# Kernel optimization log

Measured on AMD Instinct MI355X. Metric: run time of the kernel, lower is better.

Reference implementation:

```python
import jax, jax.numpy as jnp
import numpy as np

B, L, D, C, N, K = 4096, 4096, 1024, 64, 8192, 5
TEMP = 0.1
ALPHA = 2.0
EPS = 1e-12


def setup_inputs() -> dict:
    key = jax.random.key(0)
    ks = jax.random.split(key, 8)
    x = jax.random.normal(ks[0], (B, 1, L), jnp.float32)
    y = jax.random.randint(ks[1], (B,), 0, C)
    Wf = jax.random.normal(ks[2], (L, D), jnp.float32) * 0.02
    Wc = jax.random.normal(ks[3], (C, D), jnp.float32) * 0.02
    bc = jnp.zeros((C,), jnp.float32)
    supports_old = jax.random.normal(ks[4], (N, D), jnp.float32)
    scores_old = jax.nn.softmax(jax.random.normal(ks[5], (N, C), jnp.float32), axis=-1)
    labels_old = jax.nn.one_hot(jax.random.randint(ks[6], (N,), 0, C), C, dtype=jnp.float32)
    return dict(x=x, y=y, Wf=Wf, Wc=Wc, bc=bc, supports_old=supports_old,
                labels_old=labels_old, scores_old=scores_old)


def _l2n(v, axis):
    return v / jnp.maximum(jnp.linalg.norm(v, axis=axis, keepdims=True), EPS)


def _masked_mean(v, w):
    return jnp.sum(v * w) / jnp.maximum(jnp.sum(w), 1.0)


def _tta_loss(x, Wf, Wc, bc, supports_old, labels_old, scores_old):
    feats = x.reshape(B, L) @ Wf                      # [B, D] featurizer
    logits = feats @ Wc.T + bc                        # [B, C]
    probs = jax.nn.softmax(logits, -1)
    logp = jax.nn.log_softmax(logits, -1)
    prob = probs.max(-1)
    pred = jnp.argmax(logits, -1)
    # prediction-confidence filter
    y_certain = prob >= prob.mean()
    # input-energy entropy filter (scipy.stats.entropy over axis=2)
    px = x * x
    px = px / jnp.maximum(px.sum(2, keepdims=True), EPS)
    e = -(px * jnp.log(px + 1e-30)).sum(2).reshape(B)
    e_certain = e < e.mean()
    w_c = (e_certain & y_certain).astype(jnp.float32)  # certain mask as weights
    w_u = 1.0 - w_c
    yhat = jax.nn.one_hot(pred, C, dtype=jnp.float32)
    # --- memory bank concat + prototype build (no_grad in torch) ---
    sup_all = jnp.concatenate([supports_old, feats], 0)        # [N+B, D]
    lab_all = jnp.concatenate([labels_old, yhat], 0)           # [N+B, C]
    w_all = jnp.concatenate([jnp.ones((N,), jnp.float32), w_c], 0)
    lw = lab_all * w_all[:, None]
    protos = _l2n(sup_all, 1).T @ lw / jnp.maximum(lw.sum(0, keepdims=True), EPS)
    protos = jax.lax.stop_gradient(_l2n(protos, 0))            # [D, C]
    # --- loss1: Tsallis entropy - diversity on balanced probs ---
    m = jnp.sum(probs * w_c[:, None], 0) / jnp.maximum(w_c.sum(), 1.0)
    pb = probs / jnp.maximum(m, EPS)
    pb = pb / pb.sum(1, keepdims=True)
    tsallis = jnp.mean((1.0 - jnp.sum(pb ** ALPHA, 1)) / (ALPHA - 1.0))
    pm = pb.mean(0)
    div = -jnp.sum(pm * jnp.log(pm + EPS))
    loss1 = tsallis - div
    # --- loss2: PCL, prototype CE on certain samples (temp=1) ---
    lp = jax.nn.log_softmax(_l2n(feats, 1) @ protos, -1)       # [B, C]
    ce = -jnp.take_along_axis(lp, pred[:, None], 1)[:, 0]
    loss2 = _masked_mean(ce, w_c)
    # --- loss3: NCL, kNN soft targets from memory bank, uncertain rows ---
    scores_all = jax.lax.stop_gradient(jnp.concatenate([scores_old, probs], 0))
    sup_det = jax.lax.stop_gradient(sup_all)
    sim = _l2n(feats, 1) @ _l2n(sup_det, 1).T / TEMP           # [B, N+B]
    sim = jnp.where(w_all[None, :] > 0, sim, -jnp.inf)
    _, idx = jax.lax.top_k(sim, K)                             # [B, K]
    tgt = scores_all[idx].mean(1)                              # [B, C]
    ncl = -(tgt * logp).sum(1)
    loss3 = _masked_mean(ncl, w_u)
    return loss1 + loss2 + loss3


def reference(x, y, Wf, Wc, bc, supports_old, labels_old, scores_old):
    return _tta_loss(x, Wf, Wc, bc, supports_old, labels_old, scores_old)
```

## Files before the change

### kernel.cpp

```cpp
#include <hip/hip_runtime.h>
#include <math.h>

#define BBATCH 4096
#define LLEN   4096
#define DDIM   1024
#define CCLS   64
#define NSUP   8192
#define NTOT   12288
#define FEPS   1e-12f
#define KCHUNK 96
#define KCAND  (KCHUNK*5)

#define SC_SUMP  0
#define SC_SUME  1
#define SC_SUMWC 2
#define SC_TSAL  3
#define SC_L2NUM 4
#define SC_L3NUM 5

typedef _Float16 half4_t __attribute__((ext_vector_type(4)));
typedef _Float16 half8_t __attribute__((ext_vector_type(8)));
typedef float    f32x4   __attribute__((ext_vector_type(4)));
typedef float    f32x16  __attribute__((ext_vector_type(16)));

static const size_t OFF_FEATS  = 0;
static const size_t OFF_FEATP1 = OFF_FEATS  + (size_t)BBATCH*DDIM;
static const size_t OFF_WFTH   = OFF_FEATP1 + (size_t)BBATCH*DDIM;
static const size_t OFF_WFTL   = OFF_WFTH   + (size_t)DDIM*LLEN/2;
static const size_t OFF_PROBS  = OFF_WFTL   + (size_t)DDIM*LLEN/2;
static const size_t OFF_LOGP   = OFF_PROBS  + (size_t)BBATCH*CCLS;
static const size_t OFF_FNORM  = OFF_LOGP   + (size_t)BBATCH*CCLS;
static const size_t OFF_SNORM  = OFF_FNORM  + BBATCH;
static const size_t OFF_PMAX   = OFF_SNORM  + NSUP;
static const size_t OFF_EROW   = OFF_PMAX   + BBATCH;
static const size_t OFF_WC     = OFF_EROW   + BBATCH;
static const size_t OFF_PRED   = OFF_WC     + BBATCH;
static const size_t OFF_RB     = OFF_PRED   + BBATCH;
static const size_t OFF_SNM    = OFF_RB     + BBATCH;
static const size_t OFF_PROTOT = OFF_SNM    + NTOT;
static const size_t OFF_CVAL   = OFF_PROTOT + (size_t)CCLS*DDIM;
static const size_t OFF_CIDX   = OFF_CVAL   + (size_t)BBATCH*KCAND;
static const size_t OFF_ZERO   = OFF_CIDX   + (size_t)BBATCH*KCAND;
static const size_t OFF_MACC   = OFF_ZERO;
static const size_t OFF_PMACC  = OFF_MACC   + CCLS;
static const size_t OFF_COLS   = OFF_PMACC  + CCLS;
static const size_t OFF_SCAL   = OFF_COLS   + CCLS;
static const size_t OFF_PROTUN = OFF_SCAL   + 32;
static const size_t OFF_ZEND   = OFF_PROTUN + (size_t)DDIM*CCLS;
static const size_t OFF_SUPH   = OFF_ZEND;
static const size_t OFF_SUPL   = OFF_SUPH   + (size_t)NSUP*DDIM/2;
static const size_t WS_END     = OFF_SUPL   + (size_t)NSUP*DDIM/2;

__device__ __forceinline__ float waveSum(float v){
  #pragma unroll
  for (int o = 32; o > 0; o >>= 1) v += __shfl_xor(v, o);
  return v;
}
__device__ __forceinline__ float waveMax(float v){
  #pragma unroll
  for (int o = 32; o > 0; o >>= 1) v = fmaxf(v, __shfl_xor(v, o));
  return v;
}
__device__ __forceinline__ float blockSum256(float v, float* sh4){
  v = waveSum(v);
  if ((threadIdx.x & 63) == 0) sh4[threadIdx.x >> 6] = v;
  __syncthreads();
  float r = sh4[0] + sh4[1] + sh4[2] + sh4[3];
  __syncthreads();
  return r;
}
__device__ __forceinline__ void top5_insert(float* v, int* ix, float s, int si){
  bool c0 = s > v[0], c1 = s > v[1], c2 = s > v[2], c3 = s > v[3], c4 = s > v[4];
  v[4] = c4 ? (c3 ? v[3] : s) : v[4];  ix[4] = c4 ? (c3 ? ix[3] : si) : ix[4];
  v[3] = c3 ? (c2 ? v[2] : s) : v[3];  ix[3] = c3 ? (c2 ? ix[2] : si) : ix[3];
  v[2] = c2 ? (c1 ? v[1] : s) : v[2];  ix[2] = c2 ? (c1 ? ix[1] : si) : ix[2];
  v[1] = c1 ? (c0 ? v[0] : s) : v[1];  ix[1] = c1 ? (c0 ? ix[0] : si) : ix[1];
  v[0] = c0 ? s : v[0];                ix[0] = c0 ? si : ix[0];
}
__device__ __forceinline__ void split4(const float4 v, half4_t* h, half4_t* l){
  half4_t hh, ll;
  hh[0] = (_Float16)v.x; hh[1] = (_Float16)v.y; hh[2] = (_Float16)v.z; hh[3] = (_Float16)v.w;
  ll[0] = (_Float16)(v.x - (float)hh[0]);
  ll[1] = (_Float16)(v.y - (float)hh[1]);
  ll[2] = (_Float16)(v.z - (float)hh[2]);
  ll[3] = (_Float16)(v.w - (float)hh[3]);
  *h = hh; *l = ll;
}

__global__ __launch_bounds__(256)
void k_entropy(const float* __restrict__ x, float* __restrict__ e_row,
               float* __restrict__ scal){
  __shared__ __align__(16) float lx[LLEN];
  __shared__ float sh4[4];
  int row = blockIdx.x, t = threadIdx.x;
  const float4* xr = (const float4*)(x + (size_t)row * LLEN);
  float s = 0.f;
  #pragma unroll
  for (int i = 0; i < 4; ++i){
    float4 v = xr[t + 256*i];
    ((float4*)lx)[t + 256*i] = v;
    s += v.x*v.x + v.y*v.y + v.z*v.z + v.w*v.w;
  }
  s = blockSum256(s, sh4);
  float inv = 1.0f / fmaxf(s, FEPS);
  float ent = 0.f;
  #pragma unroll
  for (int i = 0; i < 4; ++i){
    float4 v = ((float4*)lx)[t + 256*i];
    float p;
    p = v.x*v.x*inv; ent -= p * logf(p + 1e-30f);
    p = v.y*v.y*inv; ent -= p * logf(p + 1e-30f);
    p = v.z*v.z*inv; ent -= p * logf(p + 1e-30f);
    p = v.w*v.w*inv; ent -= p * logf(p + 1e-30f);
  }
  ent = blockSum256(ent, sh4);
  if (t == 0){ e_row[row] = ent; atomicAdd(&scal[SC_SUME], ent); }
}

__global__ __launch_bounds__(256)
void k_wft(const float* __restrict__ Wf, unsigned short* __restrict__ WftH,
           unsigned short* __restrict__ WftL){
  __shared__ __align__(16) float ld[64*68];
  int t = threadIdx.x;
  int d0 = blockIdx.x * 64;
  int l0 = blockIdx.y * 64;
  #pragma unroll
  for (int i = 0; i < 4; ++i){
    int flat = t + 256*i;
    int l = flat >> 4, d4 = (flat & 15) * 4;
    *(float4*)&ld[l*68 + d4] = *(const float4*)(Wf + (size_t)(l0+l)*DDIM + d0 + d4);
  }
  __syncthreads();
  #pragma unroll
  for (int i = 0; i < 4; ++i){
    int flat = t + 256*i;
    int d = flat >> 4, l4 = (flat & 15) * 4;
    float4 v = make_float4(ld[(l4+0)*68 + d], ld[(l4+1)*68 + d],
                           ld[(l4+2)*68 + d], ld[(l4+3)*68 + d]);
    half4_t h, l;
    split4(v, &h, &l);
    *(half4_t*)(WftH + (size_t)(d0+d)*LLEN + l0 + l4) = h;
    *(half4_t*)(WftL + (size_t)(d0+d)*LLEN + l0 + l4) = l;
  }
}

#define LP 40
__global__ __launch_bounds__(256)
void k_feats_mfma(const float* __restrict__ X, const unsigned short* __restrict__ WftH,
                  const unsigned short* __restrict__ WftL, float* __restrict__ featp){
  __shared__ __align__(16) _Float16 lds[4*128*LP];
  _Float16* Ah = lds;
  _Float16* Al = lds + 128*LP;
  _Float16* Bh = lds + 2*128*LP;
  _Float16* Bl = lds + 3*128*LP;
  int t = threadIdx.x;
  int n0 = blockIdx.x * 128;
  int m0 = blockIdx.y * 128;
  int kz = blockIdx.z;
  int w = t >> 6, lane = t & 63;
  int wr = w >> 1, wc = w & 1;
  int lr = lane & 15, lg = lane >> 4;
  int ar = t >> 3, akq = (t & 7);
  int br = t >> 2, bk8 = (t & 3) * 8;
  f32x4 acc[4][4];
  #pragma unroll
  for (int i=0;i<4;++i){
    #pragma unroll
    for (int j=0;j<4;++j) acc[i][j] = (f32x4)(0.f);
  }
  const int kend = kz*2048 + 2048;
  float4 avs[4]; uint4 bhs[2], bls[2];
  {
    int k0 = kz*2048;
    #pragma unroll
    for (int i=0;i<4;++i)
      avs[i] = *(const float4*)(X + (size_t)(m0 + ar + 32*i)*LLEN + k0 + akq*4);
    #pragma unroll
    for (int i=0;i<2;++i){
      bhs[i] = *(const uint4*)(WftH + (size_t)(n0 + br + 64*i)*LLEN + k0 + bk8);
      bls[i] = *(const uint4*)(WftL + (size_t)(n0 + br + 64*i)*LLEN + k0 + bk8);
    }
  }
  for (int k0 = kz*2048; k0 < kend; k0 += 32){
    __syncthreads();
    #pragma unroll
    for (int i=0;i<4;++i){
      half4_t h, l;
      split4(avs[i], &h, &l);
      *(half4_t*)&Ah[(ar + 32*i)*LP + akq*4] = h;
      *(half4_t*)&Al[(ar + 32*i)*LP + akq*4] = l;
    }
    #pragma unroll
    for (int i=0;i<2;++i){
      *(uint4*)&Bh[(br + 64*i)*LP + bk8] = bhs[i];
      *(uint4*)&Bl[(br + 64*i)*LP + bk8] = bls[i];
    }
    __syncthreads();
    if (k0 + 32 < kend){
      int kn = k0 + 32;
      #pragma unroll
      for (int i=0;i<4;++i)
        avs[i] = *(const float4*)(X + (size_t)(m0 + ar + 32*i)*LLEN + kn + akq*4);
      #pragma unroll
      for (int i=0;i<2;++i){
        bhs[i] = *(const uint4*)(WftH + (size_t)(n0 + br + 64*i)*LLEN + kn + bk8);
        bls[i] = *(const uint4*)(WftL + (size_t)(n0 + br + 64*i)*LLEN + kn + bk8);
      }
    }
    half8_t ah[4], al[4], bh[4], bl[4];
    #pragma unroll
    for (int mi=0;mi<4;++mi){
      const _Float16* p = &Ah[(wr*64 + mi*16 + lr)*LP + lg*8];
      ah[mi] = *(const half8_t*)p;
      al[mi] = *(const half8_t*)(p + 128*LP);
    }
    #pragma unroll
    for (int ni=0;ni<4;++ni){
      const _Float16* p = &Bh[(wc*64 + ni*16 + lr)*LP + lg*8];
      bh[ni] = *(const half8_t*)p;
      bl[ni] = *(const half8_t*)(p + 128*LP);
    }
    #pragma unroll
    for (int mi=0;mi<4;++mi){
      #pragma unroll
      for (int ni=0;ni<4;++ni){
        acc[mi][ni] = __builtin_amdgcn_mfma_f32_16x16x32_f16(ah[mi], bh[ni], acc[mi][ni], 0,0,0);
        acc[mi][ni] = __builtin_amdgcn_mfma_f32_16x16x32_f16(ah[mi], bl[ni], acc[mi][ni], 0,0,0);
        acc[mi][ni] = __builtin_amdgcn_mfma_f32_16x16x32_f16(al[mi], bh[ni], acc[mi][ni], 0,0,0);
      }
    }
  }
  float* outp = featp + (size_t)kz * BBATCH * DDIM;
  #pragma unroll
  for (int mi=0;mi<4;++mi){
    #pragma unroll
    for (int ni=0;ni<4;++ni){
      #pragma unroll
      for (int r=0;r<4;++r){
        int row = m0 + wr*64 + mi*16 + lg*4 + r;
        int col = n0 + wc*64 + ni*16 + lr;
        outp[(size_t)row*DDIM + col] = acc[mi][ni][r];
      }
    }
  }
}

__global__ __launch_bounds__(256)
void k_supnorm(const float* __restrict__ sup, float* __restrict__ snorm,
               _Float16* __restrict__ suph, _Float16* __restrict__ supl){
  int w = threadIdx.x >> 6, lane = threadIdx.x & 63;
  int row = blockIdx.x*4 + w;
  const float4* rp = (const float4*)(sup + (size_t)row * DDIM);
  float s = 0.f;
  #pragma unroll
  for (int j=0;j<4;++j){
    float4 v = rp[lane + 64*j];
    half4_t h, l;
    split4(v, &h, &l);
    *(half4_t*)(suph + (size_t)row*DDIM + (lane + 64*j)*4) = h;
    *(half4_t*)(supl + (size_t)row*DDIM + (lane + 64*j)*4) = l;
    s += v.x*v.x+v.y*v.y+v.z*v.z+v.w*v.w;
  }
  s = waveSum(s);
  if (lane==0) snorm[row] = sqrtf(s);
}

__global__ __launch_bounds__(256)
void k_logits(float* __restrict__ feats, const float* __restrict__ featp1,
              const float* __restrict__ Wc,
              const float* __restrict__ bc, float* __restrict__ probs,
              float* __restrict__ logp, float* __restrict__ pmax,
              int* __restrict__ pred, float* __restrict__ fnorm,
              float* __restrict__ scal,
              _Float16* __restrict__ fh, _Float16* __restrict__ fl){
  __shared__ __align__(16) float f[DDIM];
  __shared__ float z[CCLS];
  __shared__ float sh4[4];
  int row = blockIdx.x, t = threadIdx.x;
  const float4* fr0 = (const float4*)(feats  + (size_t)row * DDIM);
  const float4* fr1 = (const float4*)(featp1 + (size_t)row * DDIM);
  float ss = 0.f;
  { float4 a = fr0[t], b = fr1[t];
    float4 v = make_float4(a.x+b.x, a.y+b.y, a.z+b.z, a.w+b.w);
    ((float4*)f)[t] = v;
    ((float4*)(feats + (size_t)row*DDIM))[t] = v;
    half4_t h, l;
    split4(v, &h, &l);
    *(half4_t*)(fh + (size_t)row*DDIM + t*4) = h;
    *(half4_t*)(fl + (size_t)row*DDIM + t*4) = l;
    ss += v.x*v.x+v.y*v.y+v.z*v.z+v.w*v.w; }
  ss = blockSum256(ss, sh4);
  if (t==0) fnorm[row] = sqrtf(ss);
  int w = t >> 6, lane = t & 63;
  for (int ci = 0; ci < 16; ++ci){
    int c = w*16 + ci;
    const float4* wc = (const float4*)(Wc + (size_t)c * DDIM);
    float d = 0.f;
    #pragma unroll
    for (int j=0;j<4;++j){
      float4 a = wc[lane + 64*j];
      float4 b = ((float4*)f)[lane + 64*j];
      d += a.x*b.x+a.y*b.y+a.z*b.z+a.w*b.w;
    }
    d = waveSum(d);
    if (lane == 0) z[c] = d + bc[c];
  }
  __syncthreads();
  if (w == 0){
    float zz = z[lane];
    float m = waveMax(zz);
    unsigned long long bal = __ballot(zz == m);
    int am = __ffsll(bal) - 1;
    float ex = expf(zz - m);
    float sv = waveSum(ex);
    probs[(size_t)row*CCLS + lane] = ex / sv;
    logp[(size_t)row*CCLS + lane]  = (zz - m) - logf(sv);
    if (lane == 0){
      float pmv = 1.0f / sv;
      pmax[row] = pmv;
      pred[row] = am;
      atomicAdd(&scal[SC_SUMP], pmv);
    }
  }
}

__global__ __launch_bounds__(256)
void k_mask(const float* __restrict__ e_row, const float* __restrict__ pmax,
            const float* __restrict__ fnorm, const float* __restrict__ snorm,
            const int* __restrict__ pred, float* __restrict__ w_c,
            float* __restrict__ rb, float* __restrict__ snm,
            float* __restrict__ colsum, float* __restrict__ scal){
  int i = blockIdx.x * 256 + threadIdx.x;
  if (i < NSUP) snm[i] = 1.0f / fmaxf(snorm[i], FEPS);
  if (i < BBATCH){
    float me = scal[SC_SUME] * (1.0f/BBATCH);
    float mp = scal[SC_SUMP] * (1.0f/BBATCH);
    float wc = ((e_row[i] < me) && (pmax[i] >= mp)) ? 1.0f : 0.0f;
    w_c[i] = wc;
    float fn = fmaxf(fnorm[i], FEPS);
    rb[i] = 10.0f / fn;
    snm[NSUP + i] = (wc > 0.f) ? (1.0f / fn) : -1.0f;
    atomicAdd(&scal[SC_SUMWC], wc);
    atomicAdd(&colsum[pred[i]], wc);
  }
}

__global__ __launch_bounds__(256)
void k_colsum_labels(const float* __restrict__ labels, float* __restrict__ colsum){
  int t = threadIdx.x, c = t & 63, sub = t >> 6;
  int r0 = blockIdx.x * 256;
  float s = 0.f;
  for (int i = 0; i < 64; ++i){
    int r = r0 + sub + 4*i;
    s += labels[(size_t)r*CCLS + c];
  }
  __shared__ float loc[4][64];
  loc[sub][c] = s;
  __syncthreads();
  if (sub == 0) atomicAdd(&colsum[c], loc[0][c]+loc[1][c]+loc[2][c]+loc[3][c]);
}

__global__ __launch_bounds__(256)
void k_m_accum(const float* __restrict__ probs, const float* __restrict__ w_c,
               float* __restrict__ m_acc){
  int t = threadIdx.x, c = t & 63, sub = t >> 6;
  int r0 = blockIdx.x * 64;
  float s = 0.f;
  for (int i = 0; i < 16; ++i){
    int r = r0 + sub + 4*i;
    s += probs[(size_t)r*CCLS + c] * w_c[r];
  }
  __shared__ float loc[4][64];
  loc[sub][c] = s;
  __syncthreads();
  if (sub == 0) atomicAdd(&m_acc[c], loc[0][c]+loc[1][c]+loc[2][c]+loc[3][c]);
}

__global__ __launch_bounds__(256)
void k_loss1(const float* __restrict__ probs, const float* __restrict__ m_acc,
             float* __restrict__ pm_acc, float* __restrict__ scal){
  int t = threadIdx.x, w = t >> 6, lane = t & 63;
  float swc = fmaxf(scal[SC_SUMWC], 1.0f);
  float minv = 1.0f / fmaxf(m_acc[lane] / swc, FEPS);
  float pml = 0.f, tsl = 0.f;
  int r0 = blockIdx.x * 64 + w * 16;
  for (int i = 0; i < 16; ++i){
    int r = r0 + i;
    float pb = probs[(size_t)r*CCLS + lane] * minv;
    float t1 = waveSum(pb);
    float t2 = waveSum(pb*pb);
    tsl += 1.0f - t2/(t1*t1);
    pml += pb/t1;
  }
  atomicAdd(&pm_acc[lane], pml);
  if (lane == 0) atomicAdd(&scal[SC_TSAL], tsl);
}

__global__ __launch_bounds__(256)
void k_protos_gemm(const float* __restrict__ sup, const float* __restrict__ feats,
                   const float* __restrict__ labels, const int* __restrict__ pred,
                   const float* __restrict__ w_c, const float* __restrict__ snm,
                   float* __restrict__ protos_un){
  __shared__ __align__(16) float ssx[64*68];
  __shared__ __align__(16) float sl[64*68];
  int t = threadIdx.x;
  int d0 = blockIdx.x * 64;
  int nbase = blockIdx.y * 1536;
  int dg = t & 15, cg = t >> 4;
  float acc[4][4];
  #pragma unroll
  for (int i=0;i<4;++i){
    #pragma unroll
    for (int j=0;j<4;++j) acc[i][j]=0.f;
  }
  for (int n0 = 0; n0 < 1536; n0 += 64){
    __syncthreads();
    #pragma unroll
    for (int i = 0; i < 4; ++i){
      int fidx = t + 256*i;
      int r = fidx >> 4;
      int dc = (fidx & 15) * 4;
      int n = nbase + n0 + r;
      const float* rp = (n < NSUP) ? (sup + (size_t)n*DDIM)
                                   : (feats + (size_t)(n-NSUP)*DDIM);
      *(float4*)&ssx[r*68 + dc] = *(const float4*)(rp + d0 + dc);
    }
    #pragma unroll
    for (int i = 0; i < 4; ++i){
      int fidx = t + 256*i;
      int r = fidx >> 4;
      int cc = (fidx & 15) * 4;
      int n = nbase + n0 + r;
      float sc = snm[n];
      float4 v;
      if (n < NSUP){
        float4 lb = *(const float4*)(labels + (size_t)n*CCLS + cc);
        v.x = lb.x*sc; v.y = lb.y*sc; v.z = lb.z*sc; v.w = lb.w*sc;
      } else {
        int b = n - NSUP;
        float base = w_c[b] * sc;
        int p = pred[b];
        v.x = (p == cc+0) ? base : 0.f;
        v.y = (p == cc+1) ? base : 0.f;
        v.z = (p == cc+2) ? base : 0.f;
        v.w = (p == cc+3) ? base : 0.f;
      }
      *(float4*)&sl[r*68 + cc] = v;
    }
    __syncthreads();
    #pragma unroll 4
    for (int kk = 0; kk < 64; ++kk){
      float4 a = *(float4*)&ssx[kk*68 + 4*dg];
      float4 b = *(float4*)&sl[kk*68 + 4*cg];
      float av[4] = {a.x,a.y,a.z,a.w};
      float bv[4] = {b.x,b.y,b.z,b.w};
      #pragma unroll
      for (int i=0;i<4;++i){
        #pragma unroll
        for (int j=0;j<4;++j) acc[i][j] = fmaf(av[i], bv[j], acc[i][j]);
      }
    }
  }
  #pragma unroll
  for (int i=0;i<4;++i){
    #pragma unroll
    for (int j=0;j<4;++j)
      atomicAdd(&protos_un[(size_t)(d0 + 4*dg + i)*CCLS + 4*cg + j], acc[i][j]);
  }
}

__global__ __launch_bounds__(256)
void k_protos_norm(const float* __restrict__ protos_un, const float* __restrict__ colsum,
                   float* __restrict__ protos_t){
  int c = blockIdx.x, t = threadIdx.x;
  __shared__ float sh4[4];
  float cs = fmaxf(colsum[c], FEPS);
  float v[4];
  float ss = 0.f;
  #pragma unroll
  for (int i=0;i<4;++i){
    int d = t + 256*i;
    v[i] = protos_un[(size_t)d*CCLS + c] / cs;
    ss += v[i]*v[i];
  }
  ss = blockSum256(ss, sh4);
  float inv = 1.0f / fmaxf(sqrtf(ss), FEPS);
  #pragma unroll
  for (int i=0;i<4;++i){
    int d = t + 256*i;
    protos_t[(size_t)c*DDIM + d] = v[i]*inv;
  }
}

__global__ __launch_bounds__(256)
void k_loss2(const float* __restrict__ feats, const float* __restrict__ protos_t,
             const int* __restrict__ pred, const float* __restrict__ w_c,
             const float* __restrict__ fnorm, float* __restrict__ scal){
  int row = blockIdx.x, t = threadIdx.x;
  float wc = w_c[row];
  if (wc == 0.f) return;
  __shared__ __align__(16) float f[DDIM];
  __shared__ float z[CCLS];
  float inv = 1.0f / fmaxf(fnorm[row], FEPS);
  { float4 v = ((const float4*)(feats + (size_t)row*DDIM))[t];
    v.x*=inv; v.y*=inv; v.z*=inv; v.w*=inv;
    ((float4*)f)[t] = v; }
  __syncthreads();
  int w = t >> 6, lane = t & 63;
  for (int ci=0; ci<16; ++ci){
    int c = w*16+ci;
    const float4* pc = (const float4*)(protos_t + (size_t)c*DDIM);
    float d = 0.f;
    #pragma unroll
    for (int j=0;j<4;++j){
      float4 a = pc[lane + 64*j];
      float4 b = ((float4*)f)[lane + 64*j];
      d += a.x*b.x+a.y*b.y+a.z*b.z+a.w*b.w;
    }
    d = waveSum(d);
    if (lane==0) z[c] = d;
  }
  __syncthreads();
  if (w == 0){
    float zz = z[lane];
    float m = waveMax(zz);
    float sv = waveSum(expf(zz - m));
    if (lane == 0){
      float lse = m + logf(sv);
      float ce = lse - z[pred[row]];
      atomicAdd(&scal[SC_L2NUM], ce * wc);
    }
  }
}

#define SUBH 4096
__global__ __launch_bounds__(256)
void k_sim_mfma(const _Float16* __restrict__ fh, const _Float16* __restrict__ fl,
                const _Float16* __restrict__ suph, const _Float16* __restrict__ supl,
                const float* __restrict__ rb, const float* __restrict__ snm,
                float* __restrict__ cval, int* __restrict__ cidx){
  __shared__ __align__(16) _Float16 lds[2*4*SUBH];
  __shared__ float sns[128];
  int t = threadIdx.x;
  int m0 = blockIdx.x * 128;
  int n0 = blockIdx.y * 128;
  int w = t >> 6, lane = t & 63;
  int wr = w >> 1, wc = w & 1;
  int l31 = lane & 31, hi = lane >> 5;
  if (t < 128) sns[t] = snm[m0 + t];
  const _Float16* Agh; const _Float16* Agl;
  if (blockIdx.x < 64){ Agh = suph + (size_t)m0*DDIM; Agl = supl + (size_t)m0*DDIM; }
  else                { Agh = fh + (size_t)(m0-NSUP)*DDIM; Agl = fl + (size_t)(m0-NSUP)*DDIM; }
  const _Float16* Bgh = fh + (size_t)n0*DDIM;
  const _Float16* Bgl = fl + (size_t)n0*DDIM;
  int csrc = (lane & 3) ^ ((lane >> 3) & 3);
  const size_t gl_base = (size_t)(lane >> 2) * DDIM + (size_t)csrc * 8;
  f32x16 acc[2][2];
  #pragma unroll
  for (int i=0;i<2;++i){
    #pragma unroll
    for (int j=0;j<2;++j) acc[i][j] = (f32x16)(0.f);
  }

  #define STAGE(bufi, k0c) do {                                                  \
    _Float16* Lb = lds + (bufi)*(4*SUBH);                                        \
    _Pragma("unroll")                                                            \
    for (int s2 = 0; s2 < 2; ++s2){                                              \
      int blk = s2*4 + w;                                                        \
      size_t go = gl_base + (size_t)blk*16*DDIM + (k0c);                         \
      __builtin_amdgcn_global_load_lds(                                          \
        (const __attribute__((address_space(1))) void*)(Agh + go),               \
        (__attribute__((address_space(3))) void*)(Lb + 0*SUBH + blk*512), 16,0,0);\
      __builtin_amdgcn_global_load_lds(                                          \
        (const __attribute__((address_space(1))) void*)(Agl + go),               \
        (__attribute__((address_space(3))) void*)(Lb + 1*SUBH + blk*512), 16,0,0);\
      __builtin_amdgcn_global_load_lds(                                          \
        (const __attribute__((address_space(1))) void*)(Bgh + go),               \
        (__attribute__((address_space(3))) void*)(Lb + 2*SUBH + blk*512), 16,0,0);\
      __builtin_amdgcn_global_load_lds(                                          \
        (const __attribute__((address_space(1))) void*)(Bgl + go),               \
        (__attribute__((address_space(3))) void*)(Lb + 3*SUBH + blk*512), 16,0,0);\
    }                                                                            \
  } while(0)

  STAGE(0, 0);
  __syncthreads();
  int cur = 0;
  int swz = (l31 >> 1) & 3;
  for (int it = 0; it < 32; ++it){
    if (it < 31) STAGE(cur ^ 1, (it + 1) * 32);
    const _Float16* Ah = lds + cur*(4*SUBH);
    const _Float16* Al = Ah + SUBH;
    const _Float16* Bh = Ah + 2*SUBH;
    const _Float16* Bl = Ah + 3*SUBH;
    #pragma unroll
    for (int kf = 0; kf < 2; ++kf){
      int sc = (kf*2 + hi) ^ swz;
      half8_t ahf[2], alf[2], bhf[2], blf[2];
      #pragma unroll
      for (int mi=0;mi<2;++mi){
        int off = (wr*64 + mi*32 + l31)*32 + sc*8;
        ahf[mi] = *(const half8_t*)&Ah[off];
        alf[mi] = *(const half8_t*)&Al[off];
      }
      #pragma unroll
      for (int ni=0;ni<2;++ni){
        int off = (wc*64 + ni*32 + l31)*32 + sc*8;
        bhf[ni] = *(const half8_t*)&Bh[off];
        blf[ni] = *(const half8_t*)&Bl[off];
      }
      #pragma unroll
      for (int mi=0;mi<2;++mi){
        #pragma unroll
        for (int ni=0;ni<2;++ni){
          acc[mi][ni] = __builtin_amdgcn_mfma_f32_32x32x16_f16(ahf[mi], bhf[ni], acc[mi][ni], 0,0,0);
          acc[mi][ni] = __builtin_amdgcn_mfma_f32_32x32x16_f16(ahf[mi], blf[ni], acc[mi][ni], 0,0,0);
          acc[mi][ni] = __builtin_amdgcn_mfma_f32_32x32x16_f16(alf[mi], bhf[ni], acc[mi][ni], 0,0,0);
        }
      }
    }
    __syncthreads();
    cur ^= 1;
  }
  #undef STAGE
  float tv[2][5]; int ti[2][5];
  #pragma unroll
  for (int ni=0;ni<2;++ni){
    #pragma unroll
    for (int k=0;k<5;++k){ tv[ni][k] = -INFINITY; ti[ni][k] = 0x7fffffff; }
  }
  #pragma unroll
  for (int ni=0;ni<2;++ni){
    float rbv = rb[n0 + wc*64 + ni*32 + l31];
    #pragma unroll
    for (int mi=0;mi<2;++mi){
      #pragma unroll
      for (int r=0;r<16;++r){
        int rl = wr*64 + mi*32 + (r&3) + 8*(r>>2) + 4*hi;
        float sn = sns[rl];
        float v = acc[mi][ni][r] * rbv * fabsf(sn);
        v = (sn > 0.f) ? v : -INFINITY;
        top5_insert(tv[ni], ti[ni], v, m0 + rl);
      }
    }
  }
  #pragma unroll
  for (int ni=0;ni<2;++ni){
    float pv[5]; int pi[5];
    #pragma unroll
    for (int k=0;k<5;++k){ pv[k] = __shfl_xor(tv[ni][k], 32); pi[k] = __shfl_xor(ti[ni][k], 32); }
    #pragma unroll
    for (int k=0;k<5;++k) top5_insert(tv[ni], ti[ni], pv[k], pi[k]);
  }
  __syncthreads();
  float* MV = (float*)lds;
  int*   MI = (int*)(lds + 8192);
  if (hi == 0){
    #pragma unroll
    for (int ni=0;ni<2;++ni){
      int col = wc*64 + ni*32 + l31;
      #pragma unroll
      for (int k=0;k<5;++k){
        MV[(col*2 + wr)*5 + k] = tv[ni][k];
        MI[(col*2 + wr)*5 + k] = ti[ni][k];
      }
    }
  }
  __syncthreads();
  if (t < 128){
    float bv[5]; int bi[5];
    #pragma unroll
    for (int k=0;k<5;++k){ bv[k] = MV[(t*2+0)*5 + k]; bi[k] = MI[(t*2+0)*5 + k]; }
    #pragma unroll
    for (int k=0;k<5;++k) top5_insert(bv, bi, MV[(t*2+1)*5 + k], MI[(t*2+1)*5 + k]);
    float* co = cval + (size_t)(n0 + t)*KCAND + blockIdx.x*5;
    int*   ci = cidx + (size_t)(n0 + t)*KCAND + blockIdx.x*5;
    #pragma unroll
    for (int k=0;k<5;++k){ co[k] = bv[k]; ci[k] = bi[k]; }
  }
}

__global__ __launch_bounds__(256)
void k_merge_ncl(const float* __restrict__ cval, const int* __restrict__ cidx,
                 const float* __restrict__ scores_old, const float* __restrict__ probs,
                 const float* __restrict__ logp, const float* __restrict__ w_c,
                 float* __restrict__ scal){
  int t = threadIdx.x, w = t >> 6, lane = t & 63;
  int b = blockIdx.x*4 + w;
  float bv[5]; int bi[5];
  #pragma unroll
  for (int k=0;k<5;++k){ bv[k] = -INFINITY; bi[k] = 0x7fffffff; }
  #pragma unroll
  for (int it = 0; it < 8; ++it){
    int j = lane + 64*it;
    if (j < KCAND)
      top5_insert(bv, bi, cval[(size_t)b*KCAND + j], cidx[(size_t)b*KCAND + j]);
  }
  #pragma unroll
  for (int off = 32; off > 0; off >>= 1){
    float pv[5]; int pi[5];
    #pragma unroll
    for (int k=0;k<5;++k){ pv[k] = __shfl_xor(bv[k], off); pi[k] = __shfl_xor(bi[k], off); }
    #pragma unroll
    for (int k=0;k<5;++k) top5_insert(bv, bi, pv[k], pi[k]);
  }
  float tg = 0.f;
  #pragma unroll
  for (int k=0;k<5;++k){
    int ix = bi[k];
    const float* srow = (ix < NSUP) ? (scores_old + (size_t)ix*CCLS)
                                    : (probs + (size_t)(ix-NSUP)*CCLS);
    tg += srow[lane];
  }
  tg *= 0.2f;
  float d = tg * logp[(size_t)b*CCLS + lane];
  d = waveSum(d);
  if (lane == 0) atomicAdd(&scal[SC_L3NUM], -d * (1.0f - w_c[b]));
}

__global__ void k_final(const float* __restrict__ pm_acc, const float* __restrict__ scal,
                        float* __restrict__ out){
  int lane = threadIdx.x;
  float pm = pm_acc[lane] * (1.0f/BBATCH);
  float dterm = pm * logf(pm + FEPS);
  float dv = waveSum(dterm);
  if (lane == 0){
    float div = -dv;
    float tsallis = scal[SC_TSAL] * (1.0f/BBATCH);
    float swc = scal[SC_SUMWC];
    float l1 = tsallis - div;
    float l2 = scal[SC_L2NUM] / fmaxf(swc, 1.0f);
    float l3 = scal[SC_L3NUM] / fmaxf((float)BBATCH - swc, 1.0f);
    out[0] = l1 + l2 + l3;
  }
}

extern "C" void kernel_launch(void* const* d_in, const int* in_sizes, int n_in,
                              void* d_out, int out_size, void* d_ws, size_t ws_size,
                              hipStream_t stream){
  (void)in_sizes; (void)n_in; (void)out_size; (void)ws_size;
  const float* x      = (const float*)d_in[0];
  const float* Wf     = (const float*)d_in[2];
  const float* Wc     = (const float*)d_in[3];
  const float* bc     = (const float*)d_in[4];
  const float* sup    = (const float*)d_in[5];
  const float* labels = (const float*)d_in[6];
  const float* scores = (const float*)d_in[7];
  float* ws = (float*)d_ws;

  float* feats  = ws + OFF_FEATS;
  float* featp1 = ws + OFF_FEATP1;
  unsigned short* wfth = (unsigned short*)(ws + OFF_WFTH);
  unsigned short* wftl = (unsigned short*)(ws + OFF_WFTL);
  _Float16* feat_h = (_Float16*)(ws + OFF_WFTH);
  _Float16* feat_l = (_Float16*)(ws + OFF_WFTL);
  _Float16* sup_h  = (_Float16*)(ws + OFF_SUPH);
  _Float16* sup_l  = (_Float16*)(ws + OFF_SUPL);
  float* probs  = ws + OFF_PROBS;
  float* logp   = ws + OFF_LOGP;
  float* fnorm  = ws + OFF_FNORM;
  float* snorm  = ws + OFF_SNORM;
  float* pmax   = ws + OFF_PMAX;
  float* e_row  = ws + OFF_EROW;
  float* w_c    = ws + OFF_WC;
  int*   pred   = (int*)(ws + OFF_PRED);
  float* rb     = ws + OFF_RB;
  float* snm    = ws + OFF_SNM;
  float* protot = ws + OFF_PROTOT;
  float* cvalp  = ws + OFF_CVAL;
  int*   cidxp  = (int*)(ws + OFF_CIDX);
  float* m_acc  = ws + OFF_MACC;
  float* pm_acc = ws + OFF_PMACC;
  float* colsum = ws + OFF_COLS;
  float* scal   = ws + OFF_SCAL;
  float* protun = ws + OFF_PROTUN;

  hipMemsetAsync(ws + OFF_ZERO, 0, (OFF_ZEND - OFF_ZERO)*sizeof(float), stream);

  k_entropy      <<<BBATCH, 256, 0, stream>>>(x, e_row, scal);
  k_wft          <<<dim3(DDIM/64, LLEN/64), 256, 0, stream>>>(Wf, wfth, wftl);
  k_feats_mfma   <<<dim3(DDIM/128, BBATCH/128, 2), 256, 0, stream>>>(x, wfth, wftl, feats);
  k_supnorm      <<<NSUP/4, 256, 0, stream>>>(sup, snorm, sup_h, sup_l);
  k_logits       <<<BBATCH, 256, 0, stream>>>(feats, featp1, Wc, bc, probs, logp, pmax, pred, fnorm, scal, feat_h, feat_l);
  k_mask         <<<32, 256, 0, stream>>>(e_row, pmax, fnorm, snorm, pred, w_c, rb, snm, colsum, scal);
  k_colsum_labels<<<32, 256, 0, stream>>>(labels, colsum);
  k_m_accum      <<<64, 256, 0, stream>>>(probs, w_c, m_acc);
  k_loss1        <<<64, 256, 0, stream>>>(probs, m_acc, pm_acc, scal);
  k_protos_gemm  <<<dim3(16, 8), 256, 0, stream>>>(sup, feats, labels, pred, w_c, snm, protun);
  k_protos_norm  <<<CCLS, 256, 0, stream>>>(protun, colsum, protot);
  k_loss2        <<<BBATCH, 256, 0, stream>>>(feats, protot, pred, w_c, fnorm, scal);
  k_sim_mfma     <<<dim3(KCHUNK, BBATCH/128), 256, 0, stream>>>(feat_h, feat_l, sup_h, sup_l, rb, snm, cvalp, cidxp);
  k_merge_ncl    <<<BBATCH/4, 256, 0, stream>>>(cvalp, cidxp, scores, probs, logp, w_c, scal);
  k_final        <<<1, 64, 0, stream>>>(pm_acc, scal, (float*)d_out);
}
```

Before: 1.005 ms.

## Rewrite featurizer GEMM with double-buffered LDS, direct global-to-LDS loads, 32x32 MFMA

The featurizer split-fp16 GEMM now double-buffers LDS tiles and streams the pre-split Wf halves straight into LDS with global_load_lds, so one barrier per k-step replaces two. It moves from 16x16x32 to 32x32x16 MFMA and swaps padded rows for an XOR-swizzled layout to avoid bank conflicts. The X tile is still split to hi/lo in registers. LDS use doubles, which may cut occupancy, and the swizzle and global_load_lds addressing must stay consistent.

```diff
diff --git a/kernel.cpp b/kernel.cpp
--- a/kernel.cpp
+++ b/kernel.cpp
@@ -86,6 +86,17 @@
   ll[3] = (_Float16)(v.w - (float)hh[3]);
   *h = hh; *l = ll;
 }
+__device__ __forceinline__ void split8(const float4 a, const float4 b,
+                                       half8_t* h, half8_t* l){
+  half8_t hh, ll;
+  hh[0]=(_Float16)a.x; hh[1]=(_Float16)a.y; hh[2]=(_Float16)a.z; hh[3]=(_Float16)a.w;
+  hh[4]=(_Float16)b.x; hh[5]=(_Float16)b.y; hh[6]=(_Float16)b.z; hh[7]=(_Float16)b.w;
+  ll[0]=(_Float16)(a.x-(float)hh[0]); ll[1]=(_Float16)(a.y-(float)hh[1]);
+  ll[2]=(_Float16)(a.z-(float)hh[2]); ll[3]=(_Float16)(a.w-(float)hh[3]);
+  ll[4]=(_Float16)(b.x-(float)hh[4]); ll[5]=(_Float16)(b.y-(float)hh[5]);
+  ll[6]=(_Float16)(b.z-(float)hh[6]); ll[7]=(_Float16)(b.w-(float)hh[7]);
+  *h = hh; *l = ll;
+}
 
 __global__ __launch_bounds__(256)
 void k_entropy(const float* __restrict__ x, float* __restrict__ e_row,
@@ -144,101 +155,115 @@
   }
 }
 
-#define LP 40
-__global__ __launch_bounds__(256)
-void k_feats_mfma(const float* __restrict__ X, const unsigned short* __restrict__ WftH,
-                  const unsigned short* __restrict__ WftL, float* __restrict__ featp){
-  __shared__ __align__(16) _Float16 lds[4*128*LP];
-  _Float16* Ah = lds;
-  _Float16* Al = lds + 128*LP;
-  _Float16* Bh = lds + 2*128*LP;
-  _Float16* Bl = lds + 3*128*LP;
+#define SUBH 4096
+
+__global__ __launch_bounds__(256)
+void k_feats_mfma(const float* __restrict__ X, const unsigned short* __restrict__ WftHu,
+                  const unsigned short* __restrict__ WftLu, float* __restrict__ featp){
+  __shared__ __align__(16) _Float16 lds[2*4*SUBH];
   int t = threadIdx.x;
   int n0 = blockIdx.x * 128;
   int m0 = blockIdx.y * 128;
   int kz = blockIdx.z;
   int w = t >> 6, lane = t & 63;
   int wr = w >> 1, wc = w & 1;
-  int lr = lane & 15, lg = lane >> 4;
-  int ar = t >> 3, akq = (t & 7);
-  int br = t >> 2, bk8 = (t & 3) * 8;
-  f32x4 acc[4][4];
-  #pragma unroll
-  for (int i=0;i<4;++i){
-    #pragma unroll
-    for (int j=0;j<4;++j) acc[i][j] = (f32x4)(0.f);
-  }
-  const int kend = kz*2048 + 2048;
-  float4 avs[4]; uint4 bhs[2], bls[2];
-  {
-    int k0 = kz*2048;
-    #pragma unroll
-    for (int i=0;i<4;++i)
-      avs[i] = *(const float4*)(X + (size_t)(m0 + ar + 32*i)*LLEN + k0 + akq*4);
-    #pragma unroll
-    for (int i=0;i<2;++i){
-      bhs[i] = *(const uint4*)(WftH + (size_t)(n0 + br + 64*i)*LLEN + k0 + bk8);
-      bls[i] = *(const uint4*)(WftL + (size_t)(n0 + br + 64*i)*LLEN + k0 + bk8);
-    }
-  }
-  for (int k0 = kz*2048; k0 < kend; k0 += 32){
+  int l31 = lane & 31, hi = lane >> 5;
+  const _Float16* Bgh = (const _Float16*)WftHu + (size_t)n0*LLEN;
+  const _Float16* Bgl = (const _Float16*)WftLu + (size_t)n0*LLEN;
+  int csrc = (lane & 3) ^ ((lane >> 3) & 3);
+  const size_t glB = (size_t)(lane >> 2)*LLEN + (size_t)csrc*8;
+  int ra = t >> 1;
+  int kg8 = (t & 1) * 16;
+  int aswz = (ra >> 1) & 3;
+  const float* Ag = X + (size_t)(m0 + ra)*LLEN + kg8;
+  f32x16 acc[2][2];
+  #pragma unroll
+  for (int i=0;i<2;++i){
+    #pragma unroll
+    for (int j=0;j<2;++j) acc[i][j] = (f32x16)(0.f);
+  }
+  const int kstart = kz*2048;
+
+  #define STAGE_B(bufi, k0c) do {                                                 \
+    _Float16* Lb = lds + (bufi)*(4*SUBH);                                         \
+    _Pragma("unroll")                                                             \
+    for (int s2 = 0; s2 < 2; ++s2){                                               \
+      int blk = s2*4 + w;                                                         \
+      size_t go = glB + (size_t)blk*16*LLEN + (k0c);                              \
+      __builtin_amdgcn_global_load_lds(                                           \
+        (const __attribute__((address_space(1))) void*)(Bgh + go),                \
+        (__attribute__((address_space(3))) void*)(Lb + 2*SUBH + blk*512), 16,0,0);\
+      __builtin_amdgcn_global_load_lds(                                           \
+        (const __attribute__((address_space(1))) void*)(Bgl + go),                \
+        (__attribute__((address_space(3))) void*)(Lb + 3*SUBH + blk*512), 16,0,0);\
+    }                                                                             \
+  } while(0)
+
+  STAGE_B(0, kstart);
+  float4 avs[4];
+  #pragma unroll
+  for (int i=0;i<4;++i) avs[i] = *(const float4*)(Ag + kstart + 4*i);
+  int cur = 0;
+  int swz = (l31 >> 1) & 3;
+  for (int it = 0; it < 64; ++it){
+    _Float16* Ah = lds + cur*(4*SUBH);
+    _Float16* Al = Ah + SUBH;
+    #pragma unroll
+    for (int c2 = 0; c2 < 2; ++c2){
+      half8_t hv, lv;
+      split8(avs[2*c2], avs[2*c2+1], &hv, &lv);
+      int slot = ((kg8 >> 3) + c2) ^ aswz;
+      *(half8_t*)&Ah[ra*32 + slot*8] = hv;
+      *(half8_t*)&Al[ra*32 + slot*8] = lv;
+    }
     __syncthreads();
-    #pragma unroll
-    for (int i=0;i<4;++i){
-      half4_t h, l;
-      split4(avs[i], &h, &l);
-      *(half4_t*)&Ah[(ar + 32*i)*LP + akq*4] = h;
-      *(half4_t*)&Al[(ar + 32*i)*LP + akq*4] = l;
-    }
-    #pragma unroll
-    for (int i=0;i<2;++i){
-      *(uint4*)&Bh[(br + 64*i)*LP + bk8] = bhs[i];
-      *(uint4*)&Bl[(br + 64*i)*LP + bk8] = bls[i];
-    }
-    __syncthreads();
-    if (k0 + 32 < kend){
-      int kn = k0 + 32;
-      #pragma unroll
-      for (int i=0;i<4;++i)
-        avs[i] = *(const float4*)(X + (size_t)(m0 + ar + 32*i)*LLEN + kn + akq*4);
-      #pragma unroll
-      for (int i=0;i<2;++i){
-        bhs[i] = *(const uint4*)(WftH + (size_t)(n0 + br + 64*i)*LLEN + kn + bk8);
-        bls[i] = *(const uint4*)(WftL + (size_t)(n0 + br + 64*i)*LLEN + kn + bk8);
-      }
-    }
-    half8_t ah[4], al[4], bh[4], bl[4];
-    #pragma unroll
-    for (int mi=0;mi<4;++mi){
-      const _Float16* p = &Ah[(wr*64 + mi*16 + lr)*LP + lg*8];
-      ah[mi] = *(const half8_t*)p;
-      al[mi] = *(const half8_t*)(p + 128*LP);
-    }
-    #pragma unroll
-    for (int ni=0;ni<4;++ni){
-      const _Float16* p = &Bh[(wc*64 + ni*16 + lr)*LP + lg*8];
-      bh[ni] = *(const half8_t*)p;
-      bl[ni] = *(const half8_t*)(p + 128*LP);
-    }
-    #pragma unroll
-    for (int mi=0;mi<4;++mi){
-      #pragma unroll
-      for (int ni=0;ni<4;++ni){
-        acc[mi][ni] = __builtin_amdgcn_mfma_f32_16x16x32_f16(ah[mi], bh[ni], acc[mi][ni], 0,0,0);
-        acc[mi][ni] = __builtin_amdgcn_mfma_f32_16x16x32_f16(ah[mi], bl[ni], acc[mi][ni], 0,0,0);
-        acc[mi][ni] = __builtin_amdgcn_mfma_f32_16x16x32_f16(al[mi], bh[ni], acc[mi][ni], 0,0,0);
-      }
-    }
-  }
+    if (it < 63){
+      int kn = kstart + (it+1)*32;
+      STAGE_B(cur ^ 1, kn);
+      #pragma unroll
+      for (int i=0;i<4;++i) avs[i] = *(const float4*)(Ag + kn + 4*i);
+      __builtin_amdgcn_sched_barrier(0);
+    }
+    const _Float16* Bh = lds + cur*(4*SUBH) + 2*SUBH;
+    const _Float16* Bl = Bh + SUBH;
+    #pragma unroll
+    for (int kf = 0; kf < 2; ++kf){
+      int sc = (kf*2 + hi) ^ swz;
+      half8_t ahf[2], alf[2], bhf[2], blf[2];
+      #pragma unroll
+      for (int mi=0;mi<2;++mi){
+        int off = (wr*64 + mi*32 + l31)*32 + sc*8;
+        ahf[mi] = *(const half8_t*)&Ah[off];
+        alf[mi] = *(const half8_t*)&Al[off];
+      }
+      #pragma unroll
+      for (int ni=0;ni<2;++ni){
+        int off = (wc*64 + ni*32 + l31)*32 + sc*8;
+        bhf[ni] = *(const half8_t*)&Bh[off];
+        blf[ni] = *(const half8_t*)&Bl[off];
+      }
+      #pragma unroll
+      for (int mi=0;mi<2;++mi){
+        #pragma unroll
+        for (int ni=0;ni<2;++ni){
+          acc[mi][ni] = __builtin_amdgcn_mfma_f32_32x32x16_f16(ahf[mi], bhf[ni], acc[mi][ni], 0,0,0);
+          acc[mi][ni] = __builtin_amdgcn_mfma_f32_32x32x16_f16(ahf[mi], blf[ni], acc[mi][ni], 0,0,0);
+          acc[mi][ni] = __builtin_amdgcn_mfma_f32_32x32x16_f16(alf[mi], bhf[ni], acc[mi][ni], 0,0,0);
+        }
+      }
+    }
+    cur ^= 1;
+  }
+  #undef STAGE_B
   float* outp = featp + (size_t)kz * BBATCH * DDIM;
   #pragma unroll
-  for (int mi=0;mi<4;++mi){
-    #pragma unroll
-    for (int ni=0;ni<4;++ni){
-      #pragma unroll
-      for (int r=0;r<4;++r){
-        int row = m0 + wr*64 + mi*16 + lg*4 + r;
-        int col = n0 + wc*64 + ni*16 + lr;
+  for (int mi=0;mi<2;++mi){
+    #pragma unroll
+    for (int ni=0;ni<2;++ni){
+      #pragma unroll
+      for (int r=0;r<16;++r){
+        int row = m0 + wr*64 + mi*32 + (r&3) + 8*(r>>2) + 4*hi;
+        int col = n0 + wc*64 + ni*32 + l31;
         outp[(size_t)row*DDIM + col] = acc[mi][ni][r];
       }
     }
@@ -533,7 +558,6 @@
   }
 }
 
-#define SUBH 4096
 __global__ __launch_bounds__(256)
 void k_sim_mfma(const _Float16* __restrict__ fh, const _Float16* __restrict__ fl,
                 const _Float16* __restrict__ suph, const _Float16* __restrict__ supl,
```

New measurement: 928.2 us. -7.6%, faster.
